# Kernel tuning notes

Hardware: AMD Instinct MI355X
Metric: run time of the kernel (lower is better)

Reference implementation:

```python
import jax, jax.numpy as jnp
import numpy as np

HEADS = 4
DIM_HEAD = 32


def setup_inputs() -> dict:
    key = jax.random.key(0)
    k1, k2, k3, k4 = jax.random.split(key, 4)
    b, c, H, W, D = 2, 64, 48, 48, 48
    hidden = HEADS * DIM_HEAD  # 128
    return {
        "x": jax.random.normal(k1, (b, c, H, W, D), dtype=jnp.float32),
        "W_qkv": jax.random.normal(k2, (3 * hidden, c), dtype=jnp.float32) * 0.05,
        "W_out": jax.random.normal(k3, (c, hidden), dtype=jnp.float32) * 0.05,
        "b_out": jax.random.normal(k4, (c,), dtype=jnp.float32) * 0.05,
    }


def reference(x, W_qkv, W_out, b_out):
    b, c, H, W, D = x.shape
    n = H * W * D  # flattened spatial positions
    scale = DIM_HEAD ** (-0.5)

    xf = x.reshape(b, c, n)
    # 1x1x1 conv (no bias) == channel matmul
    qkv = jnp.einsum('bcn,oc->bon', xf, W_qkv)  # [b, 3*hidden, n]
    q, k, v = jnp.split(qkv, 3, axis=1)

    def to_heads(t):
        return t.reshape(b, HEADS, DIM_HEAD, n)

    q = to_heads(q) * scale                       # [b,h,d,n]
    k = jax.nn.softmax(to_heads(k), axis=-1)      # softmax over positions
    v = to_heads(v)

    context = jnp.einsum('bhdn,bhen->bhde', k, v)  # [b,h,d,e] tiny per-head matrix
    out = jnp.einsum('bhde,bhdn->bhen', context, q)  # [b,h,e,n]
    out = out.reshape(b, HEADS * DIM_HEAD, n)

    # 1x1x1 output conv with bias
    y = jnp.einsum('bhn,oh->bon', out, W_out) + b_out[None, :, None]
    return y.reshape(b, c, H, W, D)
```

## Files before the change

kernel.cpp:

```cpp
#include <hip/hip_runtime.h>
#include <math.h>

#define CIN 64
#define NP 128

typedef float f32x4 __attribute__((ext_vector_type(4)));
typedef short s16x8 __attribute__((ext_vector_type(8)));
typedef short s16x4 __attribute__((ext_vector_type(4)));

union FragU { s16x8 v; unsigned u[4]; };
union Frag4 { s16x4 v; unsigned u[2]; };

static __device__ __forceinline__ unsigned short f2b(float f) {
    unsigned u = __builtin_bit_cast(unsigned, f);
    unsigned r = (u + 0x7FFFu + ((u >> 16) & 1u)) >> 16;
    return (unsigned short)r;
}
static __device__ __forceinline__ unsigned pack2(float lo, float hi) {
    return (unsigned)f2b(lo) | ((unsigned)f2b(hi) << 16);
}

static __device__ __forceinline__ f32x4 mfma16(s16x4 a, s16x4 b, f32x4 c) {
#if __has_builtin(__builtin_amdgcn_mfma_f32_16x16x16bf16_1k)
    return __builtin_amdgcn_mfma_f32_16x16x16bf16_1k(a, b, c, 0, 0, 0);
#else
    asm volatile("v_mfma_f32_16x16x16_bf16 %0, %1, %2, %0\n\ts_nop 7\n\ts_nop 7"
                 : "+v"(c) : "v"(a), "v"(b));
    return c;
#endif
}

__global__ __launch_bounds__(256) void prep_w(const float* __restrict__ Wqkv,
                                              unsigned short* __restrict__ Wb) {
    int e0 = (blockIdx.x * 256 + threadIdx.x) * 8;
    int lane = (e0 >> 3) & 63;
    int kc = (e0 >> 9) & 1;
    int t = e0 >> 10;
    int row = 128 + t * 16 + (lane & 15);
    int c0 = kc * 32 + (lane >> 4) * 8;
    for (int j = 0; j < 8; ++j)
        Wb[e0 + j] = f2b(Wqkv[row * 64 + c0 + j]);
}

__global__ __launch_bounds__(256, 2) void lin_attn_ctx(
    const float* __restrict__ x, const unsigned short* __restrict__ Wb,
    float* __restrict__ P, int n, int nch)
{
    __shared__ float RED[4224];

    const int tid = threadIdx.x;
    const int l = tid & 63;
    const int w = tid >> 6;
    const int h0 = blockIdx.x * 2;
    const int b = blockIdx.y;
    const int slot = blockIdx.z;
    const int nslot = gridDim.z;
    const int l15 = l & 15, lg = l >> 4;
    const uint4* Wb4 = (const uint4*)Wb;

    f32x4 zero4 = {0.f, 0.f, 0.f, 0.f};
    f32x4 ctx[2][2][2];
    float sacc[2][2] = {{0.f, 0.f}, {0.f, 0.f}};
#pragma unroll
    for (int hh = 0; hh < 2; ++hh)
#pragma unroll
        for (int a = 0; a < 2; ++a)
#pragma unroll
            for (int c2 = 0; c2 < 2; ++c2) ctx[hh][a][c2] = zero4;

    const float* xw = x + (size_t)b * CIN * n;

    for (int ch = slot; ch < nch; ch += nslot) {
        const float* xp = xw + ch * NP + w * 32 + l15;
        s16x8 bx[2][2];
#pragma unroll
        for (int pt = 0; pt < 2; ++pt)
#pragma unroll
            for (int kc = 0; kc < 2; ++kc) {
                float xv[8];
#pragma unroll
                for (int j = 0; j < 8; ++j)
                    xv[j] = xp[(size_t)(kc * 32 + lg * 8 + j) * n + pt * 16];
                FragU fu;
#pragma unroll
                for (int i = 0; i < 4; ++i)
                    fu.u[i] = pack2(xv[2 * i], xv[2 * i + 1]);
                bx[pt][kc] = fu.v;
            }

#pragma unroll
        for (int hh = 0; hh < 2; ++hh) {
            const int h = h0 + hh;
            Frag4 ekf[2][2], vf[2][2];
            {
                s16x8 ak[2][2];
#pragma unroll
                for (int rt = 0; rt < 2; ++rt)
#pragma unroll
                    for (int kc = 0; kc < 2; ++kc)
                        ak[rt][kc] = *(const s16x8*)&Wb4[((2 * h + rt) * 2 + kc) * 64 + l];
#pragma unroll
                for (int pt = 0; pt < 2; ++pt)
#pragma unroll
                    for (int rt = 0; rt < 2; ++rt) {
                        f32x4 z = zero4;
                        z = __builtin_amdgcn_mfma_f32_16x16x32_bf16(bx[pt][0], ak[rt][0], z, 0, 0, 0);
                        z = __builtin_amdgcn_mfma_f32_16x16x32_bf16(bx[pt][1], ak[rt][1], z, 0, 0, 0);
                        float e0 = __expf(z[0]), e1 = __expf(z[1]);
                        float e2 = __expf(z[2]), e3 = __expf(z[3]);
                        sacc[hh][rt] += (e0 + e1) + (e2 + e3);
                        Frag4 fe; fe.u[0] = pack2(e0, e1); fe.u[1] = pack2(e2, e3);
                        ekf[pt][rt] = fe;
                    }
            }
            __builtin_amdgcn_sched_barrier(0);
            {
                s16x8 av[2][2];
#pragma unroll
                for (int rt = 0; rt < 2; ++rt)
#pragma unroll
                    for (int kc = 0; kc < 2; ++kc)
                        av[rt][kc] = *(const s16x8*)&Wb4[((8 + 2 * h + rt) * 2 + kc) * 64 + l];
#pragma unroll
                for (int pt = 0; pt < 2; ++pt)
#pragma unroll
                    for (int rt = 0; rt < 2; ++rt) {
                        f32x4 z2 = zero4;
                        z2 = __builtin_amdgcn_mfma_f32_16x16x32_bf16(bx[pt][0], av[rt][0], z2, 0, 0, 0);
                        z2 = __builtin_amdgcn_mfma_f32_16x16x32_bf16(bx[pt][1], av[rt][1], z2, 0, 0, 0);
                        Frag4 fv; fv.u[0] = pack2(z2[0], z2[1]); fv.u[1] = pack2(z2[2], z2[3]);
                        vf[pt][rt] = fv;
                    }
            }
#pragma unroll
            for (int rt = 0; rt < 2; ++rt)
#pragma unroll
                for (int vt = 0; vt < 2; ++vt) {
                    ctx[hh][rt][vt] = mfma16(ekf[0][rt].v, vf[0][vt].v, ctx[hh][rt][vt]);
                    ctx[hh][rt][vt] = mfma16(ekf[1][rt].v, vf[1][vt].v, ctx[hh][rt][vt]);
                }
        }
    }

    float* Xf = RED;
    float* Sf = RED + 4096;
    float* Pb = P + (size_t)(b * nslot + slot) * 4224;
#pragma unroll
    for (int hh = 0; hh < 2; ++hh) {
        const int h = h0 + hh;
        __syncthreads();
#pragma unroll
        for (int rt = 0; rt < 2; ++rt)
#pragma unroll
            for (int vt = 0; vt < 2; ++vt)
#pragma unroll
                for (int r = 0; r < 4; ++r) {
                    int d = rt * 16 + lg * 4 + r, e = vt * 16 + l15;
                    Xf[w * 1024 + d * 32 + e] = ctx[hh][rt][vt][r];
                }
#pragma unroll
        for (int rt = 0; rt < 2; ++rt) {
            float s = sacc[hh][rt];
            s += __shfl_xor(s, 16);
            s += __shfl_xor(s, 32);
            if (l < 16) Sf[w * 32 + rt * 16 + l15] = s;
        }
        __syncthreads();
        for (int i = tid; i < 1024; i += 256)
            Pb[h * 1056 + i] = Xf[i] + Xf[1024 + i] + Xf[2048 + i] + Xf[3072 + i];
        if (tid < 32)
            Pb[h * 1056 + 1024 + tid] = Sf[tid] + Sf[32 + tid] + Sf[64 + tid] + Sf[96 + tid];
    }
}

__global__ __launch_bounds__(256) void reduce_p1(
    const float* __restrict__ P, float* __restrict__ P2, int nblk)
{
    const int idx = blockIdx.x * 256 + threadIdx.x;
    if (idx >= 4224) return;
    const int b = blockIdx.z, sz = blockIdx.y;
    float acc = 0.f;
    for (int slot = sz; slot < nblk; slot += 16)
        acc += P[((size_t)(b * nblk + slot)) * 4224 + idx];
    P2[((size_t)(b * 16 + sz)) * 4224 + idx] = acc;
}

__global__ __launch_bounds__(256) void reduce_p2(
    const float* __restrict__ P2, float* __restrict__ R)
{
    const int idx = blockIdx.x * 256 + threadIdx.x;
    if (idx >= 4224) return;
    const int b = blockIdx.y;
    float acc = 0.f;
#pragma unroll
    for (int s = 0; s < 16; ++s)
        acc += P2[((size_t)(b * 16 + s)) * 4224 + idx];
    R[b * 4224 + idx] = acc;
}

__global__ __launch_bounds__(256) void build_M(
    const float* __restrict__ R, const float* __restrict__ Wout,
    const float* __restrict__ Wqkv, float* __restrict__ Mt)
{
    __shared__ float ctx[4096];
    __shared__ float Ash[8 * 128];
    const int b = blockIdx.y;
    const int o0 = blockIdx.x * 8;
    const int tid = threadIdx.x;
    const float* Rb = R + b * 4224;
    for (int i = tid; i < 4096; i += 256) {
        const int hh = i >> 10, rr = i & 1023, e = rr >> 5, d = rr & 31;
        ctx[i] = Rb[hh * 1056 + d * 32 + e] / Rb[hh * 1056 + 1024 + d];
    }
    __syncthreads();
    for (int i = tid; i < 1024; i += 256) {
        const int oo = i >> 7, m = i & 127, hh = m >> 5, d = m & 31;
        float acc = 0.f;
#pragma unroll
        for (int e = 0; e < 32; ++e)
            acc += Wout[(o0 + oo) * 128 + hh * 32 + e] * ctx[hh * 1024 + e * 32 + d];
        Ash[i] = acc;
    }
    __syncthreads();
    const float scale = 0.17677669529663687f;
    for (int i = tid; i < 512; i += 256) {
        const int oo = i >> 6, c = i & 63;
        float acc = 0.f;
#pragma unroll
        for (int m = 0; m < 128; ++m)
            acc += Ash[oo * 128 + m] * Wqkv[m * 64 + c];
        Mt[b * 4096 + c * 64 + (o0 + oo)] = acc * scale;
    }
}

__global__ __launch_bounds__(256, 4) void final_proj(
    const float* __restrict__ x, const float* __restrict__ Mt,
    const float* __restrict__ bout, float* __restrict__ y, int n)
{
    const int b = blockIdx.y;
    const int p = blockIdx.x * 256 + threadIdx.x;
    const float* xb = x + (size_t)b * CIN * n + p;
    const float* M = Mt + b * 4096;
    float acc[64];
#pragma unroll
    for (int o = 0; o < 64; ++o) acc[o] = bout[o];
    for (int c = 0; c < 64; ++c) {
        const float xv = xb[(size_t)c * n];
        const float* Mr = M + c * 64;
#pragma unroll
        for (int o = 0; o < 64; ++o) acc[o] += Mr[o] * xv;
    }
    float* yb = y + (size_t)b * CIN * n + p;
#pragma unroll
    for (int o = 0; o < 64; ++o) yb[(size_t)o * n] = acc[o];
}

extern "C" void kernel_launch(void* const* d_in, const int* in_sizes, int n_in,
                              void* d_out, int out_size, void* d_ws, size_t ws_size,
                              hipStream_t stream) {
    const float* x    = (const float*)d_in[0];
    const float* Wqkv = (const float*)d_in[1];
    const float* Wout = (const float*)d_in[2];
    const float* bout = (const float*)d_in[3];
    float* y = (float*)d_out;

    const int n = in_sizes[0] / 128;
    const int nch = n / NP;

    int BLKX = 216;
    for (;;) {
        size_t need = 32768 + (size_t)2 * BLKX * 4224 * 4
                    + (size_t)2 * 16 * 4224 * 4
                    + 2 * 4224 * 4 + 2 * 4096 * 4;
        if (need <= ws_size || BLKX <= 64) break;
        BLKX >>= 1;
    }
    unsigned short* Wb = (unsigned short*)d_ws;
    float* P  = (float*)((char*)d_ws + 32768);
    float* P2 = P + (size_t)2 * BLKX * 4224;
    float* R  = P2 + (size_t)2 * 16 * 4224;
    float* Mt = R + 2 * 4224;

    prep_w<<<8, 256, 0, stream>>>(Wqkv, Wb);
    lin_attn_ctx<<<dim3(2, 2, BLKX), 256, 0, stream>>>(x, Wb, P, n, nch);
    reduce_p1<<<dim3(17, 16, 2), 256, 0, stream>>>(P, P2, BLKX);
    reduce_p2<<<dim3(17, 2), 256, 0, stream>>>(P2, R);
    build_M<<<dim3(8, 2), 256, 0, stream>>>(R, Wout, Wqkv, Mt);
    final_proj<<<dim3(n / 256, 2), 256, 0, stream>>>(x, Mt, bout, y, n);
}
```

Before: 84.40 us.

## Prefetch next x chunk into registers and fold second reduction into build_M

The context kernel now loads the next chunk's x values into registers while the current chunk's MFMA work runs, a software pipeline meant to hide global-load latency. The second-stage partial reduction kernel is removed. Each build_M block now sums the 16 partials itself into shared memory, which saves one launch and one round trip through global memory. In exchange, register pressure in the main kernel rises by 32 floats per thread, and the reduction is repeated across the 8 build_M blocks per batch.

```diff
diff --git a/kernel.cpp b/kernel.cpp
--- a/kernel.cpp
+++ b/kernel.cpp
@@ -68,25 +68,44 @@
 #pragma unroll
             for (int c2 = 0; c2 < 2; ++c2) ctx[hh][a][c2] = zero4;
 
-    const float* xw = x + (size_t)b * CIN * n;
+    const float* xw = x + (size_t)b * CIN * n + w * 32 + l15;
+
+    float xv[2][2][8];
+    {
+        const float* xp = xw + slot * NP;
+#pragma unroll
+        for (int pt = 0; pt < 2; ++pt)
+#pragma unroll
+            for (int kc = 0; kc < 2; ++kc)
+#pragma unroll
+                for (int j = 0; j < 8; ++j)
+                    xv[pt][kc][j] = xp[(size_t)(kc * 32 + lg * 8 + j) * n + pt * 16];
+    }
 
     for (int ch = slot; ch < nch; ch += nslot) {
-        const float* xp = xw + ch * NP + w * 32 + l15;
         s16x8 bx[2][2];
 #pragma unroll
         for (int pt = 0; pt < 2; ++pt)
 #pragma unroll
             for (int kc = 0; kc < 2; ++kc) {
-                float xv[8];
-#pragma unroll
-                for (int j = 0; j < 8; ++j)
-                    xv[j] = xp[(size_t)(kc * 32 + lg * 8 + j) * n + pt * 16];
                 FragU fu;
 #pragma unroll
                 for (int i = 0; i < 4; ++i)
-                    fu.u[i] = pack2(xv[2 * i], xv[2 * i + 1]);
+                    fu.u[i] = pack2(xv[pt][kc][2 * i], xv[pt][kc][2 * i + 1]);
                 bx[pt][kc] = fu.v;
             }
+
+        const int chn = ch + nslot;
+        if (chn < nch) {
+            const float* xp = xw + chn * NP;
+#pragma unroll
+            for (int pt = 0; pt < 2; ++pt)
+#pragma unroll
+                for (int kc = 0; kc < 2; ++kc)
+#pragma unroll
+                    for (int j = 0; j < 8; ++j)
+                        xv[pt][kc][j] = xp[(size_t)(kc * 32 + lg * 8 + j) * n + pt * 16];
+        }
 
 #pragma unroll
         for (int hh = 0; hh < 2; ++hh) {
@@ -185,32 +204,27 @@
     P2[((size_t)(b * 16 + sz)) * 4224 + idx] = acc;
 }
 
-__global__ __launch_bounds__(256) void reduce_p2(
-    const float* __restrict__ P2, float* __restrict__ R)
-{
-    const int idx = blockIdx.x * 256 + threadIdx.x;
-    if (idx >= 4224) return;
-    const int b = blockIdx.y;
-    float acc = 0.f;
-#pragma unroll
-    for (int s = 0; s < 16; ++s)
-        acc += P2[((size_t)(b * 16 + s)) * 4224 + idx];
-    R[b * 4224 + idx] = acc;
-}
-
 __global__ __launch_bounds__(256) void build_M(
-    const float* __restrict__ R, const float* __restrict__ Wout,
+    const float* __restrict__ P2, const float* __restrict__ Wout,
     const float* __restrict__ Wqkv, float* __restrict__ Mt)
 {
+    __shared__ float Rsh[4224];
     __shared__ float ctx[4096];
     __shared__ float Ash[8 * 128];
     const int b = blockIdx.y;
     const int o0 = blockIdx.x * 8;
     const int tid = threadIdx.x;
-    const float* Rb = R + b * 4224;
+    for (int i = tid; i < 4224; i += 256) {
+        float acc = 0.f;
+#pragma unroll
+        for (int s = 0; s < 16; ++s)
+            acc += P2[((size_t)(b * 16 + s)) * 4224 + i];
+        Rsh[i] = acc;
+    }
+    __syncthreads();
     for (int i = tid; i < 4096; i += 256) {
         const int hh = i >> 10, rr = i & 1023, e = rr >> 5, d = rr & 31;
-        ctx[i] = Rb[hh * 1056 + d * 32 + e] / Rb[hh * 1056 + 1024 + d];
+        ctx[i] = Rsh[hh * 1056 + d * 32 + e] / Rsh[hh * 1056 + 1024 + d];
     }
     __syncthreads();
     for (int i = tid; i < 1024; i += 256) {
@@ -271,20 +285,18 @@
     for (;;) {
         size_t need = 32768 + (size_t)2 * BLKX * 4224 * 4
                     + (size_t)2 * 16 * 4224 * 4
-                    + 2 * 4224 * 4 + 2 * 4096 * 4;
+                    + 2 * 4096 * 4;
         if (need <= ws_size || BLKX <= 64) break;
         BLKX >>= 1;
     }
     unsigned short* Wb = (unsigned short*)d_ws;
     float* P  = (float*)((char*)d_ws + 32768);
     float* P2 = P + (size_t)2 * BLKX * 4224;
-    float* R  = P2 + (size_t)2 * 16 * 4224;
-    float* Mt = R + 2 * 4224;
+    float* Mt = P2 + (size_t)2 * 16 * 4224;
 
     prep_w<<<8, 256, 0, stream>>>(Wqkv, Wb);
     lin_attn_ctx<<<dim3(2, 2, BLKX), 256, 0, stream>>>(x, Wb, P, n, nch);
     reduce_p1<<<dim3(17, 16, 2), 256, 0, stream>>>(P, P2, BLKX);
-    reduce_p2<<<dim3(17, 2), 256, 0, stream>>>(P2, R);
-    build_M<<<dim3(8, 2), 256, 0, stream>>>(R, Wout, Wqkv, Mt);
+    build_M<<<dim3(8, 2), 256, 0, stream>>>(P2, Wout, Wqkv, Mt);
     final_proj<<<dim3(n / 256, 2), 256, 0, stream>>>(x, Mt, bout, y, n);
 }
```

Result: slower. 87.56 us (+3.7%).
